# Optimization experiments

Measured on AMD Instinct MI355X. Metric: run time of the kernel, lower is better.

## Reference

```python
import jax, jax.numpy as jnp
import numpy as np

N_QUBITS = 13
DEPTH = 4
DIM = 2 ** N_QUBITS
PI = 3.141592653589793

# qubit 0 = most significant bit of the basis-state index
_idx = np.arange(DIM)
BITS = np.stack([(_idx >> (N_QUBITS - 1 - q)) & 1 for q in range(N_QUBITS)], axis=1)  # (DIM, n)
SIGNS = jnp.asarray(1.0 - 2.0 * BITS, dtype=jnp.float32)                               # Z eigenvalues, (DIM, n)
PARITY = jnp.asarray((-1.0) ** BITS.sum(axis=1), dtype=jnp.float32)                    # <Z^{(x)n}> diagonal, (DIM,)
# CZ entangling chain (q, q+1): diagonal (-1)^{sum_q b_q b_{q+1}}
ENT = jnp.asarray((-1.0) ** (BITS[:, :-1] * BITS[:, 1:]).sum(axis=1), dtype=jnp.float32)


def fwht(psi):
    """Normalized fast Walsh-Hadamard transform (H on every qubit), psi: (B, DIM) complex."""
    B = psi.shape[0]
    for q in range(N_QUBITS):
        psi = psi.reshape(B, 2 ** q, 2, -1)
        psi = jnp.stack([psi[:, :, 0] + psi[:, :, 1], psi[:, :, 0] - psi[:, :, 1]], axis=2)
    return psi.reshape(B, DIM) * (2.0 ** (-N_QUBITS / 2))


def feature_map_state(x):
    """Havlicek ZZ feature map: psi = D(x) H^n D(x) H^n |0...0>.
    Diagonal phase per basis state b: sum_j x_j s_j(b) + sum_{j<k} (pi-x_j)(pi-x_k) s_j(b) s_k(b)."""
    a = PI - x                                              # (B, n)
    u = x @ SIGNS.T                                         # (B, DIM)
    v = a @ SIGNS.T                                         # (B, DIM)
    phi = u + 0.5 * (v * v - jnp.sum(a * a, axis=1, keepdims=True))  # pair term via (sum)^2 trick
    d = jnp.exp(1j * phi)                                   # complex64 diagonal
    psi = jnp.full((x.shape[0], DIM), DIM ** -0.5, dtype=jnp.complex64)  # H^n |0>
    psi = fwht(d * psi)
    return d * psi


def _apply_1q(psi, U, q):
    """Apply 2x2 complex gate U to qubit q (bit-sliced)."""
    B = psi.shape[0]
    psi = psi.reshape(B, 2 ** q, 2, -1)
    a0, a1 = psi[:, :, 0], psi[:, :, 1]
    out = jnp.stack([U[0, 0] * a0 + U[0, 1] * a1, U[1, 0] * a0 + U[1, 1] * a1], axis=2)
    return out.reshape(B, DIM)


def variational_apply(psi, theta):
    """(DEPTH+1) layers of per-qubit Rz(b)Ry(a), CZ-chain entanglers between layers."""
    th = theta.reshape(DEPTH + 1, N_QUBITS, 2)
    for l in range(DEPTH + 1):
        if l > 0:
            psi = psi * ENT
        for q in range(N_QUBITS):
            ca = jnp.cos(0.5 * th[l, q, 0])
            sa = jnp.sin(0.5 * th[l, q, 0])
            em = jnp.exp(-0.5j * th[l, q, 1])
            ep = jnp.exp(0.5j * th[l, q, 1])
            U = jnp.stack([jnp.stack([em * ca, -em * sa]), jnp.stack([ep * sa, ep * ca])])
            psi = _apply_1q(psi, U, q)
    return psi


def setup_inputs() -> dict:
    key = jax.random.key(0)
    k1, k2 = jax.random.split(key)
    x = jax.random.normal(k1, (512, N_QUBITS), dtype=jnp.float32)
    theta = 0.1 * jax.random.normal(k2, ((DEPTH + 1) * N_QUBITS * 2,), dtype=jnp.float32)
    bias = jnp.zeros((1,), dtype=jnp.float32)
    return {"x": x, "theta": theta, "bias": bias}


def reference(x, theta, bias):
    psi = feature_map_state(x)
    psi = variational_apply(psi, theta)
    prob = psi.real ** 2 + psi.imag ** 2              # (B, DIM)
    logit = prob @ PARITY + bias[0]                   # (B,)
    return jnp.stack([-logit, logit], axis=1)         # two-class logits
```

## Files before the change

### kernel.cpp

```cpp
#include <hip/hip_runtime.h>
#include <hip/hip_fp16.h>

#define NQ   13
#define DIM  8192
#define PI_F 3.14159265358979323846f
#define NT   256
#define NAMP 32

__device__ __forceinline__ int lslot(int i) { return i + 2 * (i >> 5); }
#define NSLOT (DIM + 2 * (DIM >> 5))

__device__ __forceinline__ void rsincos(float x, float* s, float* c) {
  const float INV2PI = 0.15915494309189535f;
  const float TWOPI  = 6.283185307179586f;
  float r = x * INV2PI;
  r -= rintf(r);
  float ang = r * TWOPI;
  *s = __sinf(ang);
  *c = __cosf(ang);
}

__device__ __forceinline__ void waveFence() {
  __builtin_amdgcn_wave_barrier();
  __threadfence_block();
  __builtin_amdgcn_wave_barrier();
}

__device__ __forceinline__ float2 f2fma(float s, float2 a, float2 b) {
  return make_float2(fmaf(s, a.x, b.x), fmaf(s, a.y, b.y));
}
__device__ __forceinline__ float2 f2add(float2 a, float2 b) {
  return make_float2(a.x + b.x, a.y + b.y);
}
__device__ __forceinline__ float2 f2sub(float2 a, float2 b) {
  return make_float2(a.x - b.x, a.y - b.y);
}
__device__ __forceinline__ float2 cphase(float2 v, float cs, float sn) {
  return make_float2(fmaf(cs, v.x, -sn * v.y), fmaf(cs, v.y, sn * v.x));
}
__device__ __forceinline__ float2 cmul(float2 a, float2 b) {
  return make_float2(fmaf(a.x, b.x, -a.y * b.y), fmaf(a.x, b.y, a.y * b.x));
}

__device__ __forceinline__ float2 h2f(__half2 h) { return __half22float2(h); }
__device__ __forceinline__ __half2 f2h(float2 v) { return __float22half2_rn(v); }

template<int PAT>
__device__ __forceinline__ int ampIndex(int t, int j) {
  if constexpr (PAT == 0) return (t << 5) | j;
  else if constexpr (PAT == 1) return ((t >> 5) << 10) | (j << 5) | (t & 31);
  else return ((j >> 2) << 10) | (t << 2) | (j & 3);
}

template<int PAT>
__device__ __forceinline__ void buildTree(const float* __restrict__ w, float bias,
                                          int t, float* s) {
  float base = bias;
  if constexpr (PAT == 0) {
    #pragma unroll
    for (int k = 0; k < 8; k++) base += ((t >> k) & 1) ? w[5 + k] : 0.0f;
  } else if constexpr (PAT == 1) {
    #pragma unroll
    for (int k = 0; k < 5; k++) base += ((t >> k) & 1) ? w[k] : 0.0f;
    #pragma unroll
    for (int k = 0; k < 3; k++) base += ((t >> (5 + k)) & 1) ? w[10 + k] : 0.0f;
  } else {
    #pragma unroll
    for (int k = 0; k < 8; k++) base += ((t >> k) & 1) ? w[2 + k] : 0.0f;
  }
  constexpr int P[5] = { (PAT == 1) ? 5 : 0,
                         (PAT == 1) ? 6 : 1,
                         (PAT == 0) ? 2 : ((PAT == 1) ? 7 : 10),
                         (PAT == 0) ? 3 : ((PAT == 1) ? 8 : 11),
                         (PAT == 0) ? 4 : ((PAT == 1) ? 9 : 12) };
  s[0] = base;
  #pragma unroll
  for (int k = 0; k < 5; k++) {
    float wp = w[P[k]];
    #pragma unroll
    for (int m = 0; m < (1 << k); m++) s[m | (1 << k)] = s[m] + wp;
  }
}

template<int PAT>
__device__ __forceinline__ void loadAmps(const __half2* __restrict__ sAmp,
                                         int t, float2* amp) {
  #pragma unroll
  for (int j = 0; j < NAMP; j++) {
    amp[j] = h2f(sAmp[lslot(ampIndex<PAT>(t, j))]);
  }
}
template<int PAT>
__device__ __forceinline__ void storeAmps(__half2* __restrict__ sAmp,
                                          int t, const float2* amp) {
  #pragma unroll
  for (int j = 0; j < NAMP; j++) {
    sAmp[lslot(ampIndex<PAT>(t, j))] = f2h(amp[j]);
  }
}

template<int KB>
__device__ __forceinline__ void fwht_bit(float2* amp) {
  #pragma unroll
  for (int j = 0; j < NAMP; j++) if (!(j & (1 << KB))) {
    int j1 = j | (1 << KB);
    float2 a0 = amp[j], a1 = amp[j1];
    amp[j]  = f2add(a0, a1);
    amp[j1] = f2sub(a0, a1);
  }
}
__device__ __forceinline__ void fwht_all5(float2* amp) {
  fwht_bit<0>(amp); fwht_bit<1>(amp); fwht_bit<2>(amp);
  fwht_bit<3>(amp); fwht_bit<4>(amp);
}

template<int KB>
__device__ __forceinline__ void applyRy(float2* amp, float ta, float sa) {
  #pragma unroll
  for (int j = 0; j < NAMP; j++) if (!(j & (1 << KB))) {
    int j1 = j | (1 << KB);
    amp[j]  = f2fma(-ta, amp[j1], amp[j]);
    amp[j1] = f2fma( sa, amp[j],  amp[j1]);
    amp[j]  = f2fma(-ta, amp[j1], amp[j]);
  }
}

template<int PAT, bool INIT>
__device__ __forceinline__ void featureDiag(float2* amp,
                                            const float* __restrict__ wX,
                                            const float* __restrict__ wA,
                                            const float* __restrict__ cons, int t) {
  float u[NAMP], v[NAMP];
  buildTree<PAT>(wX, cons[0], t, u);
  buildTree<PAT>(wA, cons[1], t, v);
  float A2 = cons[2];
  #pragma unroll
  for (int j = 0; j < NAMP; j++) {
    float phi = u[j] + 0.5f * (v[j] * v[j] - A2);
    float sn, cs; rsincos(phi, &sn, &cs);
    if constexpr (INIT) amp[j] = make_float2(cs, sn);
    else                amp[j] = cphase(amp[j], cs, sn);
  }
}

__device__ __forceinline__ void applyDiagPT(float2* amp,
                                            const float* __restrict__ wb,
                                            const float* __restrict__ eR,
                                            const float* __restrict__ eI,
                                            float bias, int t) {
  float base = bias;
  #pragma unroll
  for (int k = 0; k < 8; k++) base += ((t >> k) & 1) ? wb[5 + k] : 0.0f;
  float2 c[NAMP];
  { float sn, cs; rsincos(base, &sn, &cs); c[0] = make_float2(cs, sn); }
  #pragma unroll
  for (int k = 0; k < 5; k++) {
    float2 e = make_float2(eR[k], eI[k]);
    #pragma unroll
    for (int m = 0; m < (1 << k); m++) c[m | (1 << k)] = cmul(c[m], e);
  }
  #pragma unroll
  for (int j = 0; j < NAMP; j++) {
    int i = ampIndex<0>(t, j);
    float sgn = (__popc(i & (i >> 1)) & 1) ? -1.0f : 1.0f;
    amp[j] = cphase(amp[j], c[j].x * sgn, c[j].y * sgn);
  }
}

__global__ __launch_bounds__(NT, 2) void qc_kernel(
    const float* __restrict__ xin,
    const float* __restrict__ thin,
    const float* __restrict__ bin,
    float* __restrict__ out) {
  __shared__ alignas(16) __half2 sAmp[NSLOT];
  __shared__ float gTA[65], gSA[65];
  __shared__ float gBbit[65];
  __shared__ float eBr[65], eBi[65];
  __shared__ float wX[13], wA[13];
  __shared__ float cons[8];
  __shared__ float red[NT / 64];

  const int t = threadIdx.x;
  const int b = blockIdx.x;

  if (t < NQ) {
    float xq = xin[b * NQ + t];
    float aq = PI_F - xq;
    wX[12 - t] = -2.0f * xq;
    wA[12 - t] = -2.0f * aq;
  }
  if (t < 65) {
    float av = thin[2 * t];
    float bv = thin[2 * t + 1];
    float ca = cosf(0.5f * av);
    float sa = sinf(0.5f * av);
    gSA[t] = sa;
    gTA[t] = sa / (1.0f + ca);
    int l = t / NQ, q = t % NQ;
    int s = l * NQ + (12 - q);
    gBbit[s] = bv;
    eBr[s] = cosf(bv);
    eBi[s] = sinf(bv);
  }
  __syncthreads();
  if (t == 0) {
    float X = 0.f, A = 0.f, A2 = 0.f;
    for (int p = 0; p < NQ; p++) {
      float xq = -0.5f * wX[p], aq = -0.5f * wA[p];
      X += xq; A += aq; A2 += aq * aq;
    }
    cons[0] = X; cons[1] = A; cons[2] = A2;
    for (int l = 0; l < 5; l++) {
      float s = 0.f;
      for (int p = 0; p < NQ; p++) s += gBbit[l * NQ + p];
      cons[3 + l] = -0.5f * s;
    }
  }
  __syncthreads();

  float2 amp[NAMP];

  featureDiag<0, true>(amp, wX, wA, cons, t);
  fwht_all5(amp);
  storeAmps<0>(sAmp, t, amp);
  waveFence();

  loadAmps<1>(sAmp, t, amp);
  fwht_all5(amp);
  storeAmps<1>(sAmp, t, amp);
  __syncthreads();

  loadAmps<2>(sAmp, t, amp);
  fwht_bit<2>(amp); fwht_bit<3>(amp); fwht_bit<4>(amp);
  featureDiag<2, false>(amp, wX, wA, cons, t);
  storeAmps<2>(sAmp, t, amp);
  __syncthreads();

  float acc = 0.0f;
  for (int l = 0; l < 5; l++) {
    const int g = l * NQ;
    loadAmps<0>(sAmp, t, amp);
    if (l > 0) applyDiagPT(amp, gBbit + (l - 1) * NQ, eBr + (l - 1) * NQ,
                           eBi + (l - 1) * NQ, cons[3 + (l - 1)], t);
    applyRy<0>(amp, gTA[g + 12], gSA[g + 12]);
    applyRy<1>(amp, gTA[g + 11], gSA[g + 11]);
    applyRy<2>(amp, gTA[g + 10], gSA[g + 10]);
    applyRy<3>(amp, gTA[g + 9],  gSA[g + 9]);
    applyRy<4>(amp, gTA[g + 8],  gSA[g + 8]);
    storeAmps<0>(sAmp, t, amp);
    waveFence();
    loadAmps<1>(sAmp, t, amp);
    applyRy<0>(amp, gTA[g + 7], gSA[g + 7]);
    applyRy<1>(amp, gTA[g + 6], gSA[g + 6]);
    applyRy<2>(amp, gTA[g + 5], gSA[g + 5]);
    applyRy<3>(amp, gTA[g + 4], gSA[g + 4]);
    applyRy<4>(amp, gTA[g + 3], gSA[g + 3]);
    storeAmps<1>(sAmp, t, amp);
    __syncthreads();
    loadAmps<2>(sAmp, t, amp);
    applyRy<2>(amp, gTA[g + 2], gSA[g + 2]);
    applyRy<3>(amp, gTA[g + 1], gSA[g + 1]);
    applyRy<4>(amp, gTA[g + 0], gSA[g + 0]);
    if (l < 4) {
      storeAmps<2>(sAmp, t, amp);
      __syncthreads();
    } else {
      #pragma unroll
      for (int j = 0; j < NAMP; j++) {
        int i = ampIndex<2>(t, j);
        float p2 = fmaf(amp[j].x, amp[j].x, amp[j].y * amp[j].y);
        acc += (__popc(i) & 1) ? -p2 : p2;
      }
    }
  }

  #pragma unroll
  for (int off = 32; off > 0; off >>= 1) acc += __shfl_down(acc, off, 64);
  if ((t & 63) == 0) red[t >> 6] = acc;
  __syncthreads();
  if (t == 0) {
    float total = red[0] + red[1] + red[2] + red[3];
    float logit = total * (1.0f / 67108864.0f) + bin[0];
    out[b * 2 + 0] = -logit;
    out[b * 2 + 1] = logit;
  }
}

extern "C" void kernel_launch(void* const* d_in, const int* in_sizes, int n_in,
                              void* d_out, int out_size, void* d_ws, size_t ws_size,
                              hipStream_t stream) {
  const float* x  = (const float*)d_in[0];
  const float* th = (const float*)d_in[1];
  const float* bi = (const float*)d_in[2];
  float* out = (float*)d_out;
  int B = in_sizes[0] / NQ;
  qc_kernel<<<B, NT, 0, stream>>>(x, th, bi, out);
}
```

Measured before the change: 96.05 us.

## Use packed half2 math for middle stages and vectorized padded LDS access

Stages 1 and 2 of the FWHT and the variational Ry gates now do their arithmetic directly in packed __half2 (hadd2/hfma2) and no longer convert to float. The shared-memory layout is re-padded (4 slots per 32) so stages 0 and 2 can use 128-bit float4 loads and stores, with a separate slot mapping for stage 1. applyDiagPT builds a 16-entry phase table plus one extra multiply, and launch bounds drop to 1 block per SM. This targets LDS instruction count and conversion overhead, but it adds half-precision rounding error in the arithmetic and may lower occupancy.

```diff
diff --git a/kernel.cpp b/kernel.cpp
--- a/kernel.cpp
+++ b/kernel.cpp
@@ -7,8 +7,14 @@
 #define NT   256
 #define NAMP 32
 
-__device__ __forceinline__ int lslot(int i) { return i + 2 * (i >> 5); }
-#define NSLOT (DIM + 2 * (DIM >> 5))
+__device__ __forceinline__ int lslot(int i) { return i + 4 * (i >> 5); }
+#define NSLOT (DIM + 4 * (DIM >> 5))
+
+__device__ __forceinline__ int base0(int t) { return 36 * t; }
+__device__ __forceinline__ int base2(int t, int g) { return 1152 * g + 4 * t + 4 * (t >> 3); }
+__device__ __forceinline__ int slot1(int t, int j) { return 1152 * (t >> 5) + 36 * j + (t & 31); }
+
+union F4H { float4 f; __half2 h[4]; };
 
 __device__ __forceinline__ void rsincos(float x, float* s, float* c) {
   const float INV2PI = 0.15915494309189535f;
@@ -42,9 +48,6 @@
   return make_float2(fmaf(a.x, b.x, -a.y * b.y), fmaf(a.x, b.y, a.y * b.x));
 }
 
-__device__ __forceinline__ float2 h2f(__half2 h) { return __half22float2(h); }
-__device__ __forceinline__ __half2 f2h(float2 v) { return __float22half2_rn(v); }
-
 template<int PAT>
 __device__ __forceinline__ int ampIndex(int t, int j) {
   if constexpr (PAT == 0) return (t << 5) | j;
@@ -59,20 +62,14 @@
   if constexpr (PAT == 0) {
     #pragma unroll
     for (int k = 0; k < 8; k++) base += ((t >> k) & 1) ? w[5 + k] : 0.0f;
-  } else if constexpr (PAT == 1) {
-    #pragma unroll
-    for (int k = 0; k < 5; k++) base += ((t >> k) & 1) ? w[k] : 0.0f;
-    #pragma unroll
-    for (int k = 0; k < 3; k++) base += ((t >> (5 + k)) & 1) ? w[10 + k] : 0.0f;
   } else {
     #pragma unroll
     for (int k = 0; k < 8; k++) base += ((t >> k) & 1) ? w[2 + k] : 0.0f;
   }
-  constexpr int P[5] = { (PAT == 1) ? 5 : 0,
-                         (PAT == 1) ? 6 : 1,
-                         (PAT == 0) ? 2 : ((PAT == 1) ? 7 : 10),
-                         (PAT == 0) ? 3 : ((PAT == 1) ? 8 : 11),
-                         (PAT == 0) ? 4 : ((PAT == 1) ? 9 : 12) };
+  constexpr int P[5] = { 0, 1,
+                         (PAT == 0) ? 2 : 10,
+                         (PAT == 0) ? 3 : 11,
+                         (PAT == 0) ? 4 : 12 };
   s[0] = base;
   #pragma unroll
   for (int k = 0; k < 5; k++) {
@@ -82,20 +79,66 @@
   }
 }
 
-template<int PAT>
-__device__ __forceinline__ void loadAmps(const __half2* __restrict__ sAmp,
-                                         int t, float2* amp) {
-  #pragma unroll
-  for (int j = 0; j < NAMP; j++) {
-    amp[j] = h2f(sAmp[lslot(ampIndex<PAT>(t, j))]);
-  }
-}
-template<int PAT>
-__device__ __forceinline__ void storeAmps(__half2* __restrict__ sAmp,
-                                          int t, const float2* amp) {
-  #pragma unroll
-  for (int j = 0; j < NAMP; j++) {
-    sAmp[lslot(ampIndex<PAT>(t, j))] = f2h(amp[j]);
+__device__ __forceinline__ void loadA0f(const __half2* __restrict__ sAmp, int t, float2* amp) {
+  const __half2* p = sAmp + base0(t);
+  #pragma unroll
+  for (int k = 0; k < 8; k++) {
+    F4H u; u.f = *reinterpret_cast<const float4*>(p + 4 * k);
+    #pragma unroll
+    for (int c = 0; c < 4; c++) amp[4 * k + c] = __half22float2(u.h[c]);
+  }
+}
+__device__ __forceinline__ void storeA0f(__half2* __restrict__ sAmp, int t, const float2* amp) {
+  __half2* p = sAmp + base0(t);
+  #pragma unroll
+  for (int k = 0; k < 8; k++) {
+    F4H u;
+    #pragma unroll
+    for (int c = 0; c < 4; c++) u.h[c] = __float22half2_rn(amp[4 * k + c]);
+    *reinterpret_cast<float4*>(p + 4 * k) = u.f;
+  }
+}
+__device__ __forceinline__ void loadA2f(const __half2* __restrict__ sAmp, int t, float2* amp) {
+  #pragma unroll
+  for (int g = 0; g < 8; g++) {
+    F4H u; u.f = *reinterpret_cast<const float4*>(sAmp + base2(t, g));
+    #pragma unroll
+    for (int c = 0; c < 4; c++) amp[4 * g + c] = __half22float2(u.h[c]);
+  }
+}
+__device__ __forceinline__ void storeA2f(__half2* __restrict__ sAmp, int t, const float2* amp) {
+  #pragma unroll
+  for (int g = 0; g < 8; g++) {
+    F4H u;
+    #pragma unroll
+    for (int c = 0; c < 4; c++) u.h[c] = __float22half2_rn(amp[4 * g + c]);
+    *reinterpret_cast<float4*>(sAmp + base2(t, g)) = u.f;
+  }
+}
+
+__device__ __forceinline__ void loadA1h(const __half2* __restrict__ sAmp, int t, __half2* amp) {
+  #pragma unroll
+  for (int j = 0; j < NAMP; j++) amp[j] = sAmp[slot1(t, j)];
+}
+__device__ __forceinline__ void storeA1h(__half2* __restrict__ sAmp, int t, const __half2* amp) {
+  #pragma unroll
+  for (int j = 0; j < NAMP; j++) sAmp[slot1(t, j)] = amp[j];
+}
+__device__ __forceinline__ void loadA2h(const __half2* __restrict__ sAmp, int t, __half2* amp) {
+  #pragma unroll
+  for (int g = 0; g < 8; g++) {
+    F4H u; u.f = *reinterpret_cast<const float4*>(sAmp + base2(t, g));
+    #pragma unroll
+    for (int c = 0; c < 4; c++) amp[4 * g + c] = u.h[c];
+  }
+}
+__device__ __forceinline__ void storeA2h(__half2* __restrict__ sAmp, int t, const __half2* amp) {
+  #pragma unroll
+  for (int g = 0; g < 8; g++) {
+    F4H u;
+    #pragma unroll
+    for (int c = 0; c < 4; c++) u.h[c] = amp[4 * g + c];
+    *reinterpret_cast<float4*>(sAmp + base2(t, g)) = u.f;
   }
 }
 
@@ -109,11 +152,6 @@
     amp[j1] = f2sub(a0, a1);
   }
 }
-__device__ __forceinline__ void fwht_all5(float2* amp) {
-  fwht_bit<0>(amp); fwht_bit<1>(amp); fwht_bit<2>(amp);
-  fwht_bit<3>(amp); fwht_bit<4>(amp);
-}
-
 template<int KB>
 __device__ __forceinline__ void applyRy(float2* amp, float ta, float sa) {
   #pragma unroll
@@ -122,6 +160,27 @@
     amp[j]  = f2fma(-ta, amp[j1], amp[j]);
     amp[j1] = f2fma( sa, amp[j],  amp[j1]);
     amp[j]  = f2fma(-ta, amp[j1], amp[j]);
+  }
+}
+
+template<int KB>
+__device__ __forceinline__ void fwht_bitH(__half2* amp) {
+  #pragma unroll
+  for (int j = 0; j < NAMP; j++) if (!(j & (1 << KB))) {
+    int j1 = j | (1 << KB);
+    __half2 a0 = amp[j], a1 = amp[j1];
+    amp[j]  = __hadd2(a0, a1);
+    amp[j1] = __hsub2(a0, a1);
+  }
+}
+template<int KB>
+__device__ __forceinline__ void applyRyH(__half2* amp, __half2 nta, __half2 sa) {
+  #pragma unroll
+  for (int j = 0; j < NAMP; j++) if (!(j & (1 << KB))) {
+    int j1 = j | (1 << KB);
+    amp[j]  = __hfma2(nta, amp[j1], amp[j]);
+    amp[j1] = __hfma2(sa,  amp[j],  amp[j1]);
+    amp[j]  = __hfma2(nta, amp[j1], amp[j]);
   }
 }
 
@@ -151,29 +210,38 @@
   float base = bias;
   #pragma unroll
   for (int k = 0; k < 8; k++) base += ((t >> k) & 1) ? wb[5 + k] : 0.0f;
-  float2 c[NAMP];
+  float2 c[16];
   { float sn, cs; rsincos(base, &sn, &cs); c[0] = make_float2(cs, sn); }
   #pragma unroll
-  for (int k = 0; k < 5; k++) {
+  for (int k = 0; k < 4; k++) {
     float2 e = make_float2(eR[k], eI[k]);
     #pragma unroll
     for (int m = 0; m < (1 << k); m++) c[m | (1 << k)] = cmul(c[m], e);
   }
   #pragma unroll
-  for (int j = 0; j < NAMP; j++) {
+  for (int j = 0; j < 16; j++) {
     int i = ampIndex<0>(t, j);
     float sgn = (__popc(i & (i >> 1)) & 1) ? -1.0f : 1.0f;
     amp[j] = cphase(amp[j], c[j].x * sgn, c[j].y * sgn);
   }
-}
-
-__global__ __launch_bounds__(NT, 2) void qc_kernel(
+  float2 e4 = make_float2(eR[4], eI[4]);
+  #pragma unroll
+  for (int j = 16; j < 32; j++) {
+    int i = ampIndex<0>(t, j);
+    float sgn = (__popc(i & (i >> 1)) & 1) ? -1.0f : 1.0f;
+    float2 cc = cmul(c[j - 16], e4);
+    amp[j] = cphase(amp[j], cc.x * sgn, cc.y * sgn);
+  }
+}
+
+__global__ __launch_bounds__(NT, 1) void qc_kernel(
     const float* __restrict__ xin,
     const float* __restrict__ thin,
     const float* __restrict__ bin,
     float* __restrict__ out) {
   __shared__ alignas(16) __half2 sAmp[NSLOT];
   __shared__ float gTA[65], gSA[65];
+  __shared__ __half2 hNTA[65], hSA[65];
   __shared__ float gBbit[65];
   __shared__ float eBr[65], eBi[65];
   __shared__ float wX[13], wA[13];
@@ -194,8 +262,11 @@
     float bv = thin[2 * t + 1];
     float ca = cosf(0.5f * av);
     float sa = sinf(0.5f * av);
+    float ta = sa / (1.0f + ca);
+    gTA[t] = ta;
     gSA[t] = sa;
-    gTA[t] = sa / (1.0f + ca);
+    hNTA[t] = __float2half2_rn(-ta);
+    hSA[t]  = __float2half2_rn(sa);
     int l = t / NQ, q = t % NQ;
     int s = l * NQ + (12 - q);
     gBbit[s] = bv;
@@ -218,60 +289,79 @@
   }
   __syncthreads();
 
-  float2 amp[NAMP];
-
-  featureDiag<0, true>(amp, wX, wA, cons, t);
-  fwht_all5(amp);
-  storeAmps<0>(sAmp, t, amp);
+  {
+    float2 amp[NAMP];
+    featureDiag<0, true>(amp, wX, wA, cons, t);
+    fwht_bit<0>(amp); fwht_bit<1>(amp); fwht_bit<2>(amp);
+    fwht_bit<3>(amp); fwht_bit<4>(amp);
+    storeA0f(sAmp, t, amp);
+  }
   waveFence();
 
-  loadAmps<1>(sAmp, t, amp);
-  fwht_all5(amp);
-  storeAmps<1>(sAmp, t, amp);
-  __syncthreads();
-
-  loadAmps<2>(sAmp, t, amp);
-  fwht_bit<2>(amp); fwht_bit<3>(amp); fwht_bit<4>(amp);
-  featureDiag<2, false>(amp, wX, wA, cons, t);
-  storeAmps<2>(sAmp, t, amp);
+  {
+    __half2 amp[NAMP];
+    loadA1h(sAmp, t, amp);
+    fwht_bitH<0>(amp); fwht_bitH<1>(amp); fwht_bitH<2>(amp);
+    fwht_bitH<3>(amp); fwht_bitH<4>(amp);
+    storeA1h(sAmp, t, amp);
+  }
+  __syncthreads();
+
+  {
+    float2 amp[NAMP];
+    loadA2f(sAmp, t, amp);
+    fwht_bit<2>(amp); fwht_bit<3>(amp); fwht_bit<4>(amp);
+    featureDiag<2, false>(amp, wX, wA, cons, t);
+    storeA2f(sAmp, t, amp);
+  }
   __syncthreads();
 
   float acc = 0.0f;
   for (int l = 0; l < 5; l++) {
     const int g = l * NQ;
-    loadAmps<0>(sAmp, t, amp);
-    if (l > 0) applyDiagPT(amp, gBbit + (l - 1) * NQ, eBr + (l - 1) * NQ,
-                           eBi + (l - 1) * NQ, cons[3 + (l - 1)], t);
-    applyRy<0>(amp, gTA[g + 12], gSA[g + 12]);
-    applyRy<1>(amp, gTA[g + 11], gSA[g + 11]);
-    applyRy<2>(amp, gTA[g + 10], gSA[g + 10]);
-    applyRy<3>(amp, gTA[g + 9],  gSA[g + 9]);
-    applyRy<4>(amp, gTA[g + 8],  gSA[g + 8]);
-    storeAmps<0>(sAmp, t, amp);
+    {
+      float2 amp[NAMP];
+      loadA0f(sAmp, t, amp);
+      if (l > 0) applyDiagPT(amp, gBbit + (l - 1) * NQ, eBr + (l - 1) * NQ,
+                             eBi + (l - 1) * NQ, cons[3 + (l - 1)], t);
+      applyRy<0>(amp, gTA[g + 12], gSA[g + 12]);
+      applyRy<1>(amp, gTA[g + 11], gSA[g + 11]);
+      applyRy<2>(amp, gTA[g + 10], gSA[g + 10]);
+      applyRy<3>(amp, gTA[g + 9],  gSA[g + 9]);
+      applyRy<4>(amp, gTA[g + 8],  gSA[g + 8]);
+      storeA0f(sAmp, t, amp);
+    }
     waveFence();
-    loadAmps<1>(sAmp, t, amp);
-    applyRy<0>(amp, gTA[g + 7], gSA[g + 7]);
-    applyRy<1>(amp, gTA[g + 6], gSA[g + 6]);
-    applyRy<2>(amp, gTA[g + 5], gSA[g + 5]);
-    applyRy<3>(amp, gTA[g + 4], gSA[g + 4]);
-    applyRy<4>(amp, gTA[g + 3], gSA[g + 3]);
-    storeAmps<1>(sAmp, t, amp);
+    {
+      __half2 amp[NAMP];
+      loadA1h(sAmp, t, amp);
+      applyRyH<0>(amp, hNTA[g + 7], hSA[g + 7]);
+      applyRyH<1>(amp, hNTA[g + 6], hSA[g + 6]);
+      applyRyH<2>(amp, hNTA[g + 5], hSA[g + 5]);
+      applyRyH<3>(amp, hNTA[g + 4], hSA[g + 4]);
+      applyRyH<4>(amp, hNTA[g + 3], hSA[g + 3]);
+      storeA1h(sAmp, t, amp);
+    }
     __syncthreads();
-    loadAmps<2>(sAmp, t, amp);
-    applyRy<2>(amp, gTA[g + 2], gSA[g + 2]);
-    applyRy<3>(amp, gTA[g + 1], gSA[g + 1]);
-    applyRy<4>(amp, gTA[g + 0], gSA[g + 0]);
-    if (l < 4) {
-      storeAmps<2>(sAmp, t, amp);
-      __syncthreads();
-    } else {
-      #pragma unroll
-      for (int j = 0; j < NAMP; j++) {
-        int i = ampIndex<2>(t, j);
-        float p2 = fmaf(amp[j].x, amp[j].x, amp[j].y * amp[j].y);
-        acc += (__popc(i) & 1) ? -p2 : p2;
+    {
+      __half2 amp[NAMP];
+      loadA2h(sAmp, t, amp);
+      applyRyH<2>(amp, hNTA[g + 2], hSA[g + 2]);
+      applyRyH<3>(amp, hNTA[g + 1], hSA[g + 1]);
+      applyRyH<4>(amp, hNTA[g + 0], hSA[g + 0]);
+      if (l < 4) {
+        storeA2h(sAmp, t, amp);
+      } else {
+        #pragma unroll
+        for (int j = 0; j < NAMP; j++) {
+          int i = ampIndex<2>(t, j);
+          float2 a = __half22float2(amp[j]);
+          float p2 = fmaf(a.x, a.x, a.y * a.y);
+          acc += (__popc(i) & 1) ? -p2 : p2;
+        }
       }
     }
+    if (l < 4) __syncthreads();
   }
 
   #pragma unroll
```

New measurement: 91.52 us. -4.7%, faster.
